# Optimization experiments

Measured on AMD Instinct MI355X. Metric: run time of the kernel, lower is better.

The kernel has to match this reference:

```python
import jax, jax.numpy as jnp
import numpy as np

N_NODES = 100000
N_EDGES = 1000000
F_DIM = 128


def setup_inputs() -> dict:
    key = jax.random.key(0)
    ks = jax.random.split(key, 12)
    s = lambda k, shape: jax.random.normal(k, shape, dtype=jnp.float32) * (1.0 / np.sqrt(shape[0]))
    return {
        "x": jax.random.normal(ks[0], (N_NODES, F_DIM), dtype=jnp.float32),
        "edge_index": jax.random.randint(ks[1], (2, N_EDGES), 0, N_NODES, dtype=jnp.int64),
        "W1": s(ks[2], (2 * F_DIM, 64)), "b1": jnp.zeros((64,), jnp.float32), "A1": s(ks[3], (2 * F_DIM, 64)),
        "W2": s(ks[4], (64, 32)), "b2": jnp.zeros((32,), jnp.float32), "A2": s(ks[5], (64, 32)),
        "W3": s(ks[6], (32, 16)), "b3": jnp.zeros((16,), jnp.float32), "A3": s(ks[7], (32, 16)),
        "Wf": s(ks[8], (16, 1)), "bf": jnp.zeros((1,), jnp.float32),
    }


def _res_block(h, W, b, A):
    # out = relu(h @ W + b); residual = h @ A (bias-free adjust); return relu(out + residual)
    out = jax.nn.relu(h @ W + b)
    return jax.nn.relu(out + h @ A)


def reference(x, edge_index, W1, b1, A1, W2, b2, A2, W3, b3, A3, Wf, bf):
    # NOTE: in the original forward, the GNN output is overwritten by data.x,
    # so the effective computation is gather -> concat -> residual MLP -> sigmoid.
    src, dst = edge_index[0], edge_index[1]
    h = jnp.concatenate([x[src], x[dst]], axis=-1)  # [E, 2F]
    h = _res_block(h, W1, b1, A1)  # [E, 64]
    h = _res_block(h, W2, b2, A2)  # [E, 32]
    h = _res_block(h, W3, b3, A3)  # [E, 16]
    return jax.nn.sigmoid(h @ Wf + bf)  # [E, 1]
```

## Files before the change

kernel.cpp:

```cpp
#include <hip/hip_runtime.h>
#include <stdint.h>
#include <stddef.h>

#define E_TOTAL 1000000
#define N_NODES 100000
#define FD      128
#define ETILE   64
#define NTILES  (E_TOTAL / ETILE)
#define GRID    768

typedef __attribute__((ext_vector_type(8))) short short8;
typedef __attribute__((ext_vector_type(4))) float f32x4;

__device__ __forceinline__ short f2bf(float f) {
  union { float f; unsigned u; } v; v.f = f;
  unsigned r = (v.u + 0x7FFFu + ((v.u >> 16) & 1u)) >> 16;
  return (short)(r & 0xFFFFu);
}

__global__ __launch_bounds__(256, 2)
void linkpred_kernel(const float* __restrict__ x,
                     const int* __restrict__ ei,
                     const float* __restrict__ W1, const float* __restrict__ b1,
                     const float* __restrict__ A1,
                     const float* __restrict__ W2, const float* __restrict__ b2,
                     const float* __restrict__ A2,
                     const float* __restrict__ W3, const float* __restrict__ b3,
                     const float* __restrict__ A3,
                     const float* __restrict__ Wf, const float* __restrict__ bfp,
                     float* __restrict__ out)
{
  __shared__ __align__(16) short H0[ETILE][264];
  __shared__ __align__(16) short H1[ETILE][72];
  __shared__ __align__(16) short H2[ETILE][40];

  const int tid  = threadIdx.x;
  const int w    = tid >> 6;
  const int lane = tid & 63;
  const int col  = lane & 15;
  const int quad = lane >> 4;

  short8 B1f[2][8];
  for (int p = 0; p < 2; ++p) {
    const int n = 16 * (w + 4 * p) + col;
    const float* src = (p == 0) ? (W1 + n) : (A1 + (n - 64));
    for (int kt = 0; kt < 8; ++kt) {
      short8 f;
      for (int j = 0; j < 8; ++j)
        f[j] = f2bf(src[(kt * 32 + quad * 8 + j) * 64]);
      B1f[p][kt] = f;
    }
  }
  short8 B2f[2][2];
  for (int p = 0; p < 2; ++p) {
    const int n = 16 * ((w & 1) + 2 * p) + col;
    const float* src = (p == 0) ? (W2 + n) : (A2 + (n - 32));
    for (int kt = 0; kt < 2; ++kt) {
      short8 f;
      for (int j = 0; j < 8; ++j)
        f[j] = f2bf(src[(kt * 32 + quad * 8 + j) * 32]);
      B2f[p][kt] = f;
    }
  }
  short8 B3f[2];
  for (int p = 0; p < 2; ++p) {
    const int n = 16 * p + col;
    const float* src = (p == 0) ? (W3 + n) : (A3 + (n - 16));
    short8 f;
    for (int j = 0; j < 8; ++j)
      f[j] = f2bf(src[(quad * 8 + j) * 16]);
    B3f[p] = f;
  }
  const float b1v = b1[16 * w + col];
  const float b2v = b2[16 * (w & 1) + col];
  const float b3v = b3[col];
  const float bfv = bfp[0];
  const float Wfv = Wf[col];
  const f32x4 zero = {0.f, 0.f, 0.f, 0.f};

  float4 ga[8], gb[8];
  auto prefetch = [&](int tile) {
    const int e0 = tile * ETILE;
#pragma unroll
    for (int it = 0; it < 8; ++it) {
      const int h    = w * 32 + it * 4 + quad;
      const int e    = h >> 1;
      const int half = h & 1;
      const int node = ei[half * E_TOTAL + e0 + e];
      const float4* s4 = ((const float4*)(x + (size_t)node * FD)) + col * 2;
      ga[it] = s4[0];
      gb[it] = s4[1];
    }
  };

  prefetch(blockIdx.x);

  for (int tile = blockIdx.x; tile < NTILES; tile += gridDim.x) {
    const int e0 = tile * ETILE;

#pragma unroll
    for (int it = 0; it < 8; ++it) {
      const int h    = w * 32 + it * 4 + quad;
      const int e    = h >> 1;
      const int half = h & 1;
      short8 s;
      s[0] = f2bf(ga[it].x); s[1] = f2bf(ga[it].y);
      s[2] = f2bf(ga[it].z); s[3] = f2bf(ga[it].w);
      s[4] = f2bf(gb[it].x); s[5] = f2bf(gb[it].y);
      s[6] = f2bf(gb[it].z); s[7] = f2bf(gb[it].w);
      *(short8*)&H0[e][half * 128 + col * 8] = s;
    }
    __syncthreads();

    const int next = tile + gridDim.x;
    if (next < NTILES) prefetch(next);

    f32x4 acc[4][2];
    for (int mt = 0; mt < 4; ++mt) { acc[mt][0] = zero; acc[mt][1] = zero; }
    for (int kt = 0; kt < 8; ++kt) {
      for (int mt = 0; mt < 4; ++mt) {
        short8 a = *(const short8*)&H0[mt * 16 + col][kt * 32 + quad * 8];
        acc[mt][0] = __builtin_amdgcn_mfma_f32_16x16x32_bf16(a, B1f[0][kt], acc[mt][0], 0, 0, 0);
        acc[mt][1] = __builtin_amdgcn_mfma_f32_16x16x32_bf16(a, B1f[1][kt], acc[mt][1], 0, 0, 0);
      }
    }
    for (int mt = 0; mt < 4; ++mt)
      for (int r = 0; r < 4; ++r) {
        float o = fmaxf(acc[mt][0][r] + b1v, 0.f);
        float h = fmaxf(o + acc[mt][1][r], 0.f);
        H1[mt * 16 + quad * 4 + r][16 * w + col] = f2bf(h);
      }
    __syncthreads();

    f32x4 acc2[2][2];
    acc2[0][0] = zero; acc2[0][1] = zero; acc2[1][0] = zero; acc2[1][1] = zero;
    for (int kt = 0; kt < 2; ++kt)
      for (int mi = 0; mi < 2; ++mi) {
        const int m = (2 * (w >> 1) + mi) * 16 + col;
        short8 a = *(const short8*)&H1[m][kt * 32 + quad * 8];
        acc2[mi][0] = __builtin_amdgcn_mfma_f32_16x16x32_bf16(a, B2f[0][kt], acc2[mi][0], 0, 0, 0);
        acc2[mi][1] = __builtin_amdgcn_mfma_f32_16x16x32_bf16(a, B2f[1][kt], acc2[mi][1], 0, 0, 0);
      }
    for (int mi = 0; mi < 2; ++mi)
      for (int r = 0; r < 4; ++r) {
        float o = fmaxf(acc2[mi][0][r] + b2v, 0.f);
        float h = fmaxf(o + acc2[mi][1][r], 0.f);
        H2[(2 * (w >> 1) + mi) * 16 + quad * 4 + r][16 * (w & 1) + col] = f2bf(h);
      }
    __syncthreads();

    f32x4 acc3[2];
    acc3[0] = zero; acc3[1] = zero;
    {
      short8 a = *(const short8*)&H2[w * 16 + col][quad * 8];
      acc3[0] = __builtin_amdgcn_mfma_f32_16x16x32_bf16(a, B3f[0], acc3[0], 0, 0, 0);
      acc3[1] = __builtin_amdgcn_mfma_f32_16x16x32_bf16(a, B3f[1], acc3[1], 0, 0, 0);
    }

#pragma unroll
    for (int r = 0; r < 4; ++r) {
      float o = fmaxf(acc3[0][r] + b3v, 0.f);
      float h = fmaxf(o + acc3[1][r], 0.f);
      float t = h * Wfv;
      t += __shfl_xor(t, 1, 16);
      t += __shfl_xor(t, 2, 16);
      t += __shfl_xor(t, 4, 16);
      t += __shfl_xor(t, 8, 16);
      if (col == r) {
        float s = bfv + t;
        out[e0 + w * 16 + quad * 4 + r] = 1.0f / (1.0f + __expf(-s));
      }
    }
  }
}

extern "C" void kernel_launch(void* const* d_in, const int* in_sizes, int n_in,
                              void* d_out, int out_size, void* d_ws, size_t ws_size,
                              hipStream_t stream) {
  const float* x   = (const float*)d_in[0];
  const int*   ei  = (const int*)d_in[1];
  const float* W1  = (const float*)d_in[2];
  const float* b1  = (const float*)d_in[3];
  const float* A1  = (const float*)d_in[4];
  const float* W2  = (const float*)d_in[5];
  const float* b2  = (const float*)d_in[6];
  const float* A2  = (const float*)d_in[7];
  const float* W3  = (const float*)d_in[8];
  const float* b3  = (const float*)d_in[9];
  const float* A3  = (const float*)d_in[10];
  const float* Wf  = (const float*)d_in[11];
  const float* bfp = (const float*)d_in[12];

  hipLaunchKernelGGL(linkpred_kernel, dim3(GRID), dim3(256), 0, stream,
                     x, ei, W1, b1, A1, W2, b2, A2, W3, b3, A3, Wf, bfp,
                     (float*)d_out);
}
```

Measured before the change: 281.7 us.

## Split gather into index prefetch and inline-asm x loads, pipelined a tile ahead

Edge-index loads are now issued two tiles ahead and the x row gathers one tile ahead, using inline asm global loads so the compiler cannot insert early waits. A single vmcnt(0) wait is placed just before conversion to LDS. The layer-1 and layer-2 MFMA loops are reordered to finish one M-tile at a time, which reduces the number of live accumulators, and the grid grows from 768 to 1024 blocks. The aim is deeper memory-latency hiding for the random gathers, at the cost of more registers and reliance on hand-placed waitcnt ordering.

```diff
diff --git a/kernel.cpp b/kernel.cpp
--- a/kernel.cpp
+++ b/kernel.cpp
@@ -7,9 +7,10 @@
 #define FD      128
 #define ETILE   64
 #define NTILES  (E_TOTAL / ETILE)
-#define GRID    768
+#define GRID    1024
 
 typedef __attribute__((ext_vector_type(8))) short short8;
+typedef __attribute__((ext_vector_type(4))) int   i32x4;
 typedef __attribute__((ext_vector_type(4))) float f32x4;
 
 __device__ __forceinline__ short f2bf(float f) {
@@ -78,75 +79,86 @@
   const float Wfv = Wf[col];
   const f32x4 zero = {0.f, 0.f, 0.f, 0.f};
 
-  float4 ga[8], gb[8];
-  auto prefetch = [&](int tile) {
+  int   nd[8];
+  i32x4 gA[8], gB[8];
+
+  auto load_ei = [&](int tile) {
     const int e0 = tile * ETILE;
 #pragma unroll
     for (int it = 0; it < 8; ++it) {
-      const int h    = w * 32 + it * 4 + quad;
-      const int e    = h >> 1;
-      const int half = h & 1;
-      const int node = ei[half * E_TOTAL + e0 + e];
-      const float4* s4 = ((const float4*)(x + (size_t)node * FD)) + col * 2;
-      ga[it] = s4[0];
-      gb[it] = s4[1];
+      const int h = w * 32 + it * 4 + quad;
+      nd[it] = ei[(h & 1) * E_TOTAL + e0 + (h >> 1)];
     }
   };
-
-  prefetch(blockIdx.x);
-
-  for (int tile = blockIdx.x; tile < NTILES; tile += gridDim.x) {
-    const int e0 = tile * ETILE;
-
+  auto xissue = [&]() {
+#pragma unroll
+    for (int it = 0; it < 8; ++it) {
+      const float* p = x + (size_t)nd[it] * FD + col * 8;
+      asm volatile("global_load_dwordx4 %0, %2, off\n\t"
+                   "global_load_dwordx4 %1, %2, off offset:16"
+                   : "=&v"(gA[it]), "=&v"(gB[it]) : "v"(p) : "memory");
+    }
+  };
+  auto commit = [&]() {
+    asm volatile("s_waitcnt vmcnt(0)" ::: "memory");
+    __builtin_amdgcn_sched_barrier(0);
 #pragma unroll
     for (int it = 0; it < 8; ++it) {
       const int h    = w * 32 + it * 4 + quad;
       const int e    = h >> 1;
       const int half = h & 1;
       short8 s;
-      s[0] = f2bf(ga[it].x); s[1] = f2bf(ga[it].y);
-      s[2] = f2bf(ga[it].z); s[3] = f2bf(ga[it].w);
-      s[4] = f2bf(gb[it].x); s[5] = f2bf(gb[it].y);
-      s[6] = f2bf(gb[it].z); s[7] = f2bf(gb[it].w);
+      s[0] = f2bf(__int_as_float(gA[it][0])); s[1] = f2bf(__int_as_float(gA[it][1]));
+      s[2] = f2bf(__int_as_float(gA[it][2])); s[3] = f2bf(__int_as_float(gA[it][3]));
+      s[4] = f2bf(__int_as_float(gB[it][0])); s[5] = f2bf(__int_as_float(gB[it][1]));
+      s[6] = f2bf(__int_as_float(gB[it][2])); s[7] = f2bf(__int_as_float(gB[it][3]));
       *(short8*)&H0[e][half * 128 + col * 8] = s;
     }
+  };
+
+  load_ei(blockIdx.x);
+  xissue();
+  if (blockIdx.x + (int)gridDim.x < NTILES) load_ei(blockIdx.x + gridDim.x);
+
+  for (int tile = blockIdx.x; tile < NTILES; tile += gridDim.x) {
+    const int e0 = tile * ETILE;
+
+    commit();
     __syncthreads();
 
-    const int next = tile + gridDim.x;
-    if (next < NTILES) prefetch(next);
-
-    f32x4 acc[4][2];
-    for (int mt = 0; mt < 4; ++mt) { acc[mt][0] = zero; acc[mt][1] = zero; }
-    for (int kt = 0; kt < 8; ++kt) {
-      for (int mt = 0; mt < 4; ++mt) {
+    const int nx = tile + gridDim.x;
+    if (nx < NTILES) xissue();
+    if (nx + (int)gridDim.x < NTILES) load_ei(nx + gridDim.x);
+
+    for (int mt = 0; mt < 4; ++mt) {
+      f32x4 a0 = zero, a1 = zero;
+      for (int kt = 0; kt < 8; ++kt) {
         short8 a = *(const short8*)&H0[mt * 16 + col][kt * 32 + quad * 8];
-        acc[mt][0] = __builtin_amdgcn_mfma_f32_16x16x32_bf16(a, B1f[0][kt], acc[mt][0], 0, 0, 0);
-        acc[mt][1] = __builtin_amdgcn_mfma_f32_16x16x32_bf16(a, B1f[1][kt], acc[mt][1], 0, 0, 0);
-      }
-    }
-    for (int mt = 0; mt < 4; ++mt)
+        a0 = __builtin_amdgcn_mfma_f32_16x16x32_bf16(a, B1f[0][kt], a0, 0, 0, 0);
+        a1 = __builtin_amdgcn_mfma_f32_16x16x32_bf16(a, B1f[1][kt], a1, 0, 0, 0);
+      }
       for (int r = 0; r < 4; ++r) {
-        float o = fmaxf(acc[mt][0][r] + b1v, 0.f);
-        float h = fmaxf(o + acc[mt][1][r], 0.f);
+        float o = fmaxf(a0[r] + b1v, 0.f);
+        float h = fmaxf(o + a1[r], 0.f);
         H1[mt * 16 + quad * 4 + r][16 * w + col] = f2bf(h);
       }
+    }
     __syncthreads();
 
-    f32x4 acc2[2][2];
-    acc2[0][0] = zero; acc2[0][1] = zero; acc2[1][0] = zero; acc2[1][1] = zero;
-    for (int kt = 0; kt < 2; ++kt)
-      for (int mi = 0; mi < 2; ++mi) {
-        const int m = (2 * (w >> 1) + mi) * 16 + col;
+    for (int mi = 0; mi < 2; ++mi) {
+      f32x4 a0 = zero, a1 = zero;
+      const int m = (2 * (w >> 1) + mi) * 16 + col;
+      for (int kt = 0; kt < 2; ++kt) {
         short8 a = *(const short8*)&H1[m][kt * 32 + quad * 8];
-        acc2[mi][0] = __builtin_amdgcn_mfma_f32_16x16x32_bf16(a, B2f[0][kt], acc2[mi][0], 0, 0, 0);
-        acc2[mi][1] = __builtin_amdgcn_mfma_f32_16x16x32_bf16(a, B2f[1][kt], acc2[mi][1], 0, 0, 0);
-      }
-    for (int mi = 0; mi < 2; ++mi)
+        a0 = __builtin_amdgcn_mfma_f32_16x16x32_bf16(a, B2f[0][kt], a0, 0, 0, 0);
+        a1 = __builtin_amdgcn_mfma_f32_16x16x32_bf16(a, B2f[1][kt], a1, 0, 0, 0);
+      }
       for (int r = 0; r < 4; ++r) {
-        float o = fmaxf(acc2[mi][0][r] + b2v, 0.f);
-        float h = fmaxf(o + acc2[mi][1][r], 0.f);
+        float o = fmaxf(a0[r] + b2v, 0.f);
+        float h = fmaxf(o + a1[r], 0.f);
         H2[(2 * (w >> 1) + mi) * 16 + quad * 4 + r][16 * (w & 1) + col] = f2bf(h);
       }
+    }
     __syncthreads();
 
     f32x4 acc3[2];
```

New measurement: 284.4 us. Within noise of the previous version (+1.0%).
